# Performance work log

Measured on AMD Instinct MI355X. Metric: run time of the kernel, lower is better.

## Reference

```python
import jax, jax.numpy as jnp
import numpy as np

B, H, D = 2048, 4, 4096   # batch, num_heads_h, dim
M = 8                      # groups_m

def setup_inputs() -> dict:
    key = jax.random.key(0)
    ks = jax.random.split(key, 5)
    return {
        "x": jax.random.normal(ks[0], (B, H, D), dtype=jnp.float32),
        "local_W": jax.random.normal(ks[1], (M, H), dtype=jnp.float32) * 0.5,
        "local_b": jax.random.normal(ks[2], (M,), dtype=jnp.float32) * 0.02,
        "proj_W": jax.random.normal(ks[3], (D, D), dtype=jnp.float32) * 0.02,
        "proj_b": jax.random.normal(ks[4], (D,), dtype=jnp.float32) * 0.02,
    }

def reference(x, local_W, local_b, proj_W, proj_b):
    b, h, d = x.shape
    m = local_W.shape[0]
    dm = d // m
    # s: (m, B, dm, h)  -- matches reshape(B,h,m,-1).permute(2,0,3,1)
    s = jnp.transpose(x.reshape(b, h, m, dm), (2, 0, 3, 1))
    # grouped tiny linear (Linear(h,1) per group), all fused in one einsum
    s_out = jnp.einsum('mbch,mh->mbc', s, local_W) + local_b[:, None, None]
    # faithful to torch: cat along dim 0 then reshape(B, D) (group-major flatten)
    s_out = s_out.reshape(b, d)
    out = jax.nn.sigmoid(s_out @ proj_W.T + proj_b)
    return out
```

## Files before the change

### kernel.cpp

```cpp
#include <hip/hip_runtime.h>


#define MD 2048
#define ND 4096
#define KD 4096

typedef __attribute__((ext_vector_type(8))) __bf16 bf16x8;
typedef __attribute__((ext_vector_type(4))) float f32x4;

static __device__ __forceinline__ unsigned int f2bf(float f) {
  union { float f; unsigned int u; } v; v.f = f;
  unsigned int u = v.u;
  u += 0x7FFFu + ((u >> 16) & 1u);
  return u >> 16;
}

__global__ __launch_bounds__(256) void prep_kernel(
    const float* __restrict__ x, const float* __restrict__ lW,
    const float* __restrict__ lb, unsigned short* __restrict__ sB) {
  int g = blockIdx.x * 256 + threadIdx.x;
  int j8 = g << 3;
  int r = j8 >> 12;
  int j = j8 & 4095;
  int m = r >> 8;
  int b = ((r & 255) << 3) + (j >> 9);
  int c = j & 511;
  const float* xp = x + ((long)b << 14) + m * 512 + c;
  float w0 = lW[m * 4 + 0], w1 = lW[m * 4 + 1], w2 = lW[m * 4 + 2], w3 = lW[m * 4 + 3];
  float bb = lb[m];
  float4 xa0 = *(const float4*)(xp);
  float4 xb0 = *(const float4*)(xp + 4);
  float4 xa1 = *(const float4*)(xp + 4096);
  float4 xb1 = *(const float4*)(xp + 4100);
  float4 xa2 = *(const float4*)(xp + 8192);
  float4 xb2 = *(const float4*)(xp + 8196);
  float4 xa3 = *(const float4*)(xp + 12288);
  float4 xb3 = *(const float4*)(xp + 12292);
  float v0 = bb + xa0.x * w0 + xa1.x * w1 + xa2.x * w2 + xa3.x * w3;
  float v1 = bb + xa0.y * w0 + xa1.y * w1 + xa2.y * w2 + xa3.y * w3;
  float v2 = bb + xa0.z * w0 + xa1.z * w1 + xa2.z * w2 + xa3.z * w3;
  float v3 = bb + xa0.w * w0 + xa1.w * w1 + xa2.w * w2 + xa3.w * w3;
  float v4 = bb + xb0.x * w0 + xb1.x * w1 + xb2.x * w2 + xb3.x * w3;
  float v5 = bb + xb0.y * w0 + xb1.y * w1 + xb2.y * w2 + xb3.y * w3;
  float v6 = bb + xb0.z * w0 + xb1.z * w1 + xb2.z * w2 + xb3.z * w3;
  float v7 = bb + xb0.w * w0 + xb1.w * w1 + xb2.w * w2 + xb3.w * w3;
  uint4 pk;
  pk.x = f2bf(v0) | (f2bf(v1) << 16);
  pk.y = f2bf(v2) | (f2bf(v3) << 16);
  pk.z = f2bf(v4) | (f2bf(v5) << 16);
  pk.w = f2bf(v6) | (f2bf(v7) << 16);
  *(uint4*)(sB + j8) = pk;
}

#define BM 128
#define BN 128
#define BK 64

__global__ __launch_bounds__(256) void gemm_kernel(
    const unsigned short* __restrict__ S, const float* __restrict__ W,
    const float* __restrict__ pb, float* __restrict__ out) {
  __shared__ unsigned short As[BM * BK];
  __shared__ unsigned short Bs[BN * BK];
  __shared__ float B32[BN * BK];
  int tid = threadIdx.x;
  int lane = tid & 63;
  int wave = tid >> 6;
  int n0 = blockIdx.x * BN;
  int r0 = blockIdx.y * BM;
  int wr = wave >> 1, wc = wave & 1;

  int srow = (wave << 5) + (lane >> 3);
  int scol = (((lane & 7) ^ (lane >> 3)) << 3);
  const unsigned short* gA = S + (long)(r0 + srow) * KD + scol;
  unsigned short* lA = &As[(wave << 5) * BK];

  const float* Wn0 = W + (long)n0 * KD;
  int boff[8];
#pragma unroll
  for (int i = 0; i < 8; ++i) {
    int c = (i << 8) + tid;
    int row = c >> 4;
    boff[i] = row * KD + (((c & 15) ^ (row & 15)) << 2);
  }

  int brow = tid >> 1;
  int bh8 = (tid & 1) << 3;
  int bswz15 = brow & 15;
  int bswz7 = brow & 7;
  const float* rB32 = B32 + brow * BK;
  unsigned short* wBs = &Bs[brow * BK];

  f32x4 acc[4][4] = {};

#pragma unroll
  for (int i = 0; i < 8; ++i)
    __builtin_amdgcn_global_load_lds(
        (const __attribute__((address_space(1))) unsigned int*)(Wn0 + boff[i]),
        (__attribute__((address_space(3))) unsigned int*)(B32 + (((i << 8) + (wave << 6)) << 2)),
        16, 0, 0);

  for (int kt = 0; kt < KD; kt += BK) {
    __syncthreads();
#pragma unroll
    for (int i = 0; i < 4; ++i)
      __builtin_amdgcn_global_load_lds(
          (const __attribute__((address_space(1))) unsigned int*)(gA + (long)i * 8 * KD + kt),
          (__attribute__((address_space(3))) unsigned int*)(lA + i * 8 * BK), 16, 0, 0);
#pragma unroll
    for (int qq = 0; qq < 4; ++qq) {
      int q0 = 2 * qq, q1 = 2 * qq + 1;
      f32x4 u = *(const f32x4*)(rB32 + (((bh8 + q0) ^ bswz15) << 2));
      f32x4 v = *(const f32x4*)(rB32 + (((bh8 + q1) ^ bswz15) << 2));
      uint4 pk;
      pk.x = f2bf(u[0]) | (f2bf(u[1]) << 16);
      pk.y = f2bf(u[2]) | (f2bf(u[3]) << 16);
      pk.z = f2bf(v[0]) | (f2bf(v[1]) << 16);
      pk.w = f2bf(v[2]) | (f2bf(v[3]) << 16);
      *(uint4*)&wBs[((((bh8 >> 1) + qq) ^ bswz7) << 3)] = pk;
    }
    __syncthreads();
    if (kt + BK < KD) {
      int ktn = kt + BK;
#pragma unroll
      for (int i = 0; i < 8; ++i)
        __builtin_amdgcn_global_load_lds(
            (const __attribute__((address_space(1))) unsigned int*)(Wn0 + boff[i] + ktn),
            (__attribute__((address_space(3))) unsigned int*)(B32 + (((i << 8) + (wave << 6)) << 2)),
            16, 0, 0);
    }
#pragma unroll
    for (int ks = 0; ks < 2; ++ks) {
      int swz = (((ks << 2) + (lane >> 4)) ^ (lane & 7)) << 3;
      bf16x8 af[4], bfr[4];
#pragma unroll
      for (int t = 0; t < 4; ++t) {
        af[t]  = *(const bf16x8*)&As[((wr << 6) + t * 16 + (lane & 15)) * BK + swz];
        bfr[t] = *(const bf16x8*)&Bs[((wc << 6) + t * 16 + (lane & 15)) * BK + swz];
      }
#pragma unroll
      for (int mt = 0; mt < 4; ++mt)
#pragma unroll
        for (int nt = 0; nt < 4; ++nt)
          acc[mt][nt] = __builtin_amdgcn_mfma_f32_16x16x32_bf16(af[mt], bfr[nt], acc[mt][nt], 0, 0, 0);
    }
  }

#pragma unroll
  for (int nt = 0; nt < 4; ++nt) {
    int col = n0 + (wc << 6) + nt * 16 + (lane & 15);
    float pbv = pb[col];
#pragma unroll
    for (int mt = 0; mt < 4; ++mt) {
      int row = r0 + (wr << 6) + mt * 16 + ((lane >> 4) << 2);
#pragma unroll
      for (int i = 0; i < 4; ++i) {
        float v = acc[mt][nt][i] + pbv;
        out[(long)(row + i) * ND + col] = 1.0f / (1.0f + __expf(-v));
      }
    }
  }
}

extern "C" void kernel_launch(void* const* d_in, const int* in_sizes, int n_in,
                              void* d_out, int out_size, void* d_ws, size_t ws_size,
                              hipStream_t stream) {
  const float* x  = (const float*)d_in[0];
  const float* lW = (const float*)d_in[1];
  const float* lb = (const float*)d_in[2];
  const float* pW = (const float*)d_in[3];
  const float* pb = (const float*)d_in[4];
  float* out = (float*)d_out;

  unsigned short* sB = (unsigned short*)d_ws;

  prep_kernel<<<4096, 256, 0, stream>>>(x, lW, lb, sB);
  gemm_kernel<<<dim3(32, 16), 256, 0, stream>>>(sB, pW, pb, out);
}
```

Before: 348.3 us.

## Double-buffer GEMM tiles and stage fp32 weights through registers

The GEMM now double-buffers the bf16 A and B tiles in LDS, which lets it drop one of the two barriers per K iteration. The fp32 weight tile no longer goes through an LDS staging buffer; it is prefetched straight into registers and converted to bf16 with the native cast. The goal is to cut LDS traffic, barrier stalls and the cost of the manual rounding. In exchange the kernel uses more registers (32 floats of prefetch per thread), which may lower occupancy, and the weight loads become per-thread 128-byte strided reads.

```diff
diff --git a/kernel.cpp b/kernel.cpp
--- a/kernel.cpp
+++ b/kernel.cpp
@@ -13,6 +13,12 @@
   unsigned int u = v.u;
   u += 0x7FFFu + ((u >> 16) & 1u);
   return u >> 16;
+}
+
+static __device__ __forceinline__ unsigned int pk2bf(float a, float b) {
+  union { __bf16 h; unsigned short u; } x, y;
+  x.h = (__bf16)a; y.h = (__bf16)b;
+  return (unsigned)x.u | ((unsigned)y.u << 16);
 }
 
 __global__ __launch_bounds__(256) void prep_kernel(
@@ -59,9 +65,8 @@
 __global__ __launch_bounds__(256) void gemm_kernel(
     const unsigned short* __restrict__ S, const float* __restrict__ W,
     const float* __restrict__ pb, float* __restrict__ out) {
-  __shared__ unsigned short As[BM * BK];
-  __shared__ unsigned short Bs[BN * BK];
-  __shared__ float B32[BN * BK];
+  __shared__ unsigned short As[2][BM * BK];
+  __shared__ unsigned short Bs[2][BN * BK];
   int tid = threadIdx.x;
   int lane = tid & 63;
   int wave = tid >> 6;
@@ -72,61 +77,52 @@
   int srow = (wave << 5) + (lane >> 3);
   int scol = (((lane & 7) ^ (lane >> 3)) << 3);
   const unsigned short* gA = S + (long)(r0 + srow) * KD + scol;
-  unsigned short* lA = &As[(wave << 5) * BK];
-
-  const float* Wn0 = W + (long)n0 * KD;
-  int boff[8];
-#pragma unroll
-  for (int i = 0; i < 8; ++i) {
-    int c = (i << 8) + tid;
-    int row = c >> 4;
-    boff[i] = row * KD + (((c & 15) ^ (row & 15)) << 2);
-  }
+  int lAoff = (wave << 5) * BK;
 
   int brow = tid >> 1;
-  int bh8 = (tid & 1) << 3;
-  int bswz15 = brow & 15;
-  int bswz7 = brow & 7;
-  const float* rB32 = B32 + brow * BK;
-  unsigned short* wBs = &Bs[brow * BK];
+  int bk0 = (tid & 1) << 5;
+  const float* gW = W + (long)(n0 + brow) * KD + bk0;
+  unsigned short* bs0 = &Bs[0][brow * BK];
+  unsigned short* bs1 = &Bs[1][brow * BK];
+  int bsw = brow & 7;
+  int kcb = (tid & 1) << 2;
 
   f32x4 acc[4][4] = {};
+  f32x4 wv[8];
 
 #pragma unroll
-  for (int i = 0; i < 8; ++i)
+  for (int i = 0; i < 4; ++i)
     __builtin_amdgcn_global_load_lds(
-        (const __attribute__((address_space(1))) unsigned int*)(Wn0 + boff[i]),
-        (__attribute__((address_space(3))) unsigned int*)(B32 + (((i << 8) + (wave << 6)) << 2)),
-        16, 0, 0);
+        (const __attribute__((address_space(1))) unsigned int*)(gA + (long)i * 8 * KD),
+        (__attribute__((address_space(3))) unsigned int*)(&As[0][lAoff + i * 8 * BK]), 16, 0, 0);
+#pragma unroll
+  for (int q = 0; q < 8; ++q)
+    wv[q] = *(const f32x4*)(gW + q * 4);
 
   for (int kt = 0; kt < KD; kt += BK) {
-    __syncthreads();
+    int cur = (kt >> 6) & 1;
+    unsigned short* bs = cur ? bs1 : bs0;
 #pragma unroll
-    for (int i = 0; i < 4; ++i)
-      __builtin_amdgcn_global_load_lds(
-          (const __attribute__((address_space(1))) unsigned int*)(gA + (long)i * 8 * KD + kt),
-          (__attribute__((address_space(3))) unsigned int*)(lA + i * 8 * BK), 16, 0, 0);
-#pragma unroll
-    for (int qq = 0; qq < 4; ++qq) {
-      int q0 = 2 * qq, q1 = 2 * qq + 1;
-      f32x4 u = *(const f32x4*)(rB32 + (((bh8 + q0) ^ bswz15) << 2));
-      f32x4 v = *(const f32x4*)(rB32 + (((bh8 + q1) ^ bswz15) << 2));
+    for (int q2 = 0; q2 < 4; ++q2) {
+      f32x4 u = wv[2 * q2], v = wv[2 * q2 + 1];
       uint4 pk;
-      pk.x = f2bf(u[0]) | (f2bf(u[1]) << 16);
-      pk.y = f2bf(u[2]) | (f2bf(u[3]) << 16);
-      pk.z = f2bf(v[0]) | (f2bf(v[1]) << 16);
-      pk.w = f2bf(v[2]) | (f2bf(v[3]) << 16);
-      *(uint4*)&wBs[((((bh8 >> 1) + qq) ^ bswz7) << 3)] = pk;
+      pk.x = pk2bf(u[0], u[1]);
+      pk.y = pk2bf(u[2], u[3]);
+      pk.z = pk2bf(v[0], v[1]);
+      pk.w = pk2bf(v[2], v[3]);
+      *(uint4*)&bs[((kcb + q2) ^ bsw) << 3] = pk;
     }
     __syncthreads();
     if (kt + BK < KD) {
-      int ktn = kt + BK;
+      int nxt = cur ^ 1;
 #pragma unroll
-      for (int i = 0; i < 8; ++i)
+      for (int i = 0; i < 4; ++i)
         __builtin_amdgcn_global_load_lds(
-            (const __attribute__((address_space(1))) unsigned int*)(Wn0 + boff[i] + ktn),
-            (__attribute__((address_space(3))) unsigned int*)(B32 + (((i << 8) + (wave << 6)) << 2)),
-            16, 0, 0);
+            (const __attribute__((address_space(1))) unsigned int*)(gA + (long)i * 8 * KD + kt + BK),
+            (__attribute__((address_space(3))) unsigned int*)(&As[nxt][lAoff + i * 8 * BK]), 16, 0, 0);
+#pragma unroll
+      for (int q = 0; q < 8; ++q)
+        wv[q] = *(const f32x4*)(gW + kt + BK + q * 4);
     }
 #pragma unroll
     for (int ks = 0; ks < 2; ++ks) {
@@ -134,8 +130,8 @@
       bf16x8 af[4], bfr[4];
 #pragma unroll
       for (int t = 0; t < 4; ++t) {
-        af[t]  = *(const bf16x8*)&As[((wr << 6) + t * 16 + (lane & 15)) * BK + swz];
-        bfr[t] = *(const bf16x8*)&Bs[((wc << 6) + t * 16 + (lane & 15)) * BK + swz];
+        af[t]  = *(const bf16x8*)&As[cur][((wr << 6) + t * 16 + (lane & 15)) * BK + swz];
+        bfr[t] = *(const bf16x8*)&Bs[cur][((wc << 6) + t * 16 + (lane & 15)) * BK + swz];
       }
 #pragma unroll
       for (int mt = 0; mt < 4; ++mt)
```

Result: slower. 379.7 us (+9.0%).
